# Optimization experiments

Hardware: AMD Instinct MI355X
Metric: run time of the kernel (lower is better)

Reference implementation:

```python
import jax, jax.numpy as jnp
import numpy as np

RADIUS = 8
NUM_CORNERS = 500


def _dwconv(x, k2d, mode):
    # depthwise 2D conv on NCHW with explicit border padding (kornia-style)
    ph, pw = k2d.shape[0] // 2, k2d.shape[1] // 2
    xp = jnp.pad(x, ((0, 0), (0, 0), (ph, ph), (pw, pw)), mode=mode)
    C = x.shape[1]
    kern = jnp.broadcast_to(k2d[None, None], (C, 1, k2d.shape[0], k2d.shape[1])).astype(x.dtype)
    return jax.lax.conv_general_dilated(xp, kern, (1, 1), 'VALID',
                                        feature_group_count=C,
                                        dimension_numbers=('NCHW', 'OIHW', 'NCHW'))


def _gauss2d(k, sigma):
    x = jnp.arange(k, dtype=jnp.float32) - (k - 1) / 2.0
    g = jnp.exp(-(x * x) / (2.0 * sigma * sigma))
    g = g / g.sum()
    return jnp.outer(g, g)


def _nms2d(x):
    # kornia.feature.nms2d with (5,5) window: keep values equal to local max
    m = jax.lax.reduce_window(x, -jnp.inf, jax.lax.max, (1, 1, 5, 5), (1, 1, 1, 1), 'SAME')
    return x * (x == m).astype(x.dtype)


def _gftt(gray):
    # kornia CornerGFTT: sobel gradients (normalized /8, replicate pad),
    # structure tensor blurred with gaussian(7, sigma=1), min eigenvalue
    kx = jnp.array([[-1., 0., 1.], [-2., 0., 2.], [-1., 0., 1.]], jnp.float32) / 8.0
    dx = _dwconv(gray, kx, 'edge')
    dy = _dwconv(gray, kx.T, 'edge')
    g7 = _gauss2d(7, 1.0)
    dx2 = _dwconv(dx * dx, g7, 'reflect')
    dy2 = _dwconv(dy * dy, g7, 'reflect')
    dxy = _dwconv(dx * dy, g7, 'reflect')
    det = dx2 * dy2 - dxy * dxy
    tr = dx2 + dy2
    return 0.5 * (tr - jnp.sqrt(jnp.abs(tr * tr - 4.0 * det)))


def _laplacian5(x):
    # kornia laplacian kernel size 5, normalized by abs-sum (=48), reflect pad
    k = jnp.ones((5, 5), jnp.float32).at[2, 2].set(1.0 - 25.0)
    k = k / jnp.abs(k).sum()
    return _dwconv(x, k, 'reflect')


def _get_corners(imgs):
    B, _, H, W = imgs.shape
    r, N = RADIUS, NUM_CORNERS
    gray = 0.299 * imgs[:, :1] + 0.587 * imgs[:, 1:2] + 0.114 * imgs[:, 2:3]
    corners = _nms2d(_gftt(gray))
    # MaxPool2d(r, return_indices) + MaxUnpool2d(r): keep only per-block max
    blocks = corners.reshape(B, 1, H // r, r, W // r, r)
    bmax = blocks.max(axis=(3, 5), keepdims=True)
    unpooled = jnp.where(blocks == bmax, blocks, 0.0).reshape(B, 1, H, W)
    values, idx = jax.lax.top_k(unpooled.reshape(B, -1), N)   # [B,N]
    h, w = idx // W, idx % W
    b = jnp.repeat(jnp.arange(B), N)
    target = jnp.zeros((B, 1, H, W), imgs.dtype).at[b, 0, h.ravel(), w.ravel()].set(values.ravel())
    target = _nms2d(target)
    return (target > 0).astype(target.dtype)


def setup_inputs() -> dict:
    key = jax.random.key(0)
    k1, k2 = jax.random.split(key)
    scores_dense = jax.random.uniform(k1, (16, 1, 512, 512), dtype=jnp.float32)
    imgs = jax.random.uniform(k2, (16, 3, 512, 512), dtype=jnp.float32)
    return {"scores_dense": scores_dense, "imgs": imgs}


def reference(scores_dense, imgs):
    corners = _dwconv(_get_corners(imgs), _gauss2d(7, 1.0), 'reflect')
    lap = _laplacian5(scores_dense)
    logp = jnp.clip(jnp.log(scores_dense), -100.0)      # torch BCELoss clamps log at -100
    log1mp = jnp.clip(jnp.log1p(-scores_dense), -100.0)
    bce = -(corners * logp + (1.0 - corners) * log1mp).mean()
    return bce + (scores_dense * jnp.exp(-lap)).mean() * 10.0
```

## Files before the change

kernel.cpp:

```cpp
#include <hip/hip_runtime.h>
#include <math.h>

#define BB 16
#define HH 512
#define WW 512
#define HWP (HH*WW)
#define NPIX (BB*HWP)
#define HWP4 (HWP/4)
#define NG (NPIX/4)
#define NCORN 500
#define NSLOT 4096
#define OCAP 1024
#define NKEY (NSLOT+OCAP)
#define NKPT (NKEY/256)
#define NBL 4096

__device__ __constant__ float G7c[7] = {
    0.0044330482f, 0.0540055826f, 0.2420362294f, 0.3990502793f,
    0.2420362294f, 0.0540055826f, 0.0044330482f};

__device__ __forceinline__ int reflect_idx(int i, int n) {
    if (i < 0) i = -i;
    if (i >= n) i = 2 * n - 2 - i;
    return i;
}

__device__ __forceinline__ float w1d(int p, int o, int n) {
    float w = 0.f;
    int d = p - o;
    if (d >= -3 && d <= 3) w += G7c[d + 3];
    if (p >= 1 && p + o <= 3) w += G7c[3 - p - o];
    if (p <= n - 2 && p + o >= 2 * n - 5) w += G7c[2 * n + 1 - p - o];
    return w;
}

__global__ void k_gray(const float* __restrict__ imgs, float* __restrict__ gray) {
    int g = blockIdx.x * blockDim.x + threadIdx.x;
    if (g >= NG) return;
    int b = g / HWP4, r = g % HWP4;
    const float4* base = (const float4*)(imgs + (size_t)b * 3 * HWP);
    float4 R = base[r], G = base[r + HWP4], Bc = base[r + 2 * HWP4];
    float4 o;
    o.x = 0.299f * R.x + 0.587f * G.x + 0.114f * Bc.x;
    o.y = 0.299f * R.y + 0.587f * G.y + 0.114f * Bc.y;
    o.z = 0.299f * R.z + 0.587f * G.z + 0.114f * Bc.z;
    o.w = 0.299f * R.w + 0.587f * G.w + 0.114f * Bc.w;
    ((float4*)gray)[g] = o;
}

__global__ void k_gradH(const float* __restrict__ gray,
                        float* __restrict__ ha, float* __restrict__ hc,
                        float* __restrict__ hd) {
    int g = blockIdx.x * blockDim.x + threadIdx.x;
    if (g >= NG) return;
    int b = g / HWP4, rem = g % HWP4;
    int p = rem * 4, y = p >> 9, x0 = p & 511;
    const float* gb = gray + (size_t)b * HWP;
    int ym = max(y - 1, 0), yp = min(y + 1, HH - 1);
    const float* rm = gb + (size_t)ym * WW;
    const float* rc = gb + (size_t)y * WW;
    const float* rp = gb + (size_t)yp * WW;
    if (x0 >= 4 && x0 <= 504) {
        float r0[12], r1[12], r2[12];
        const float4* q0 = (const float4*)(rm + x0 - 4);
        const float4* q1 = (const float4*)(rc + x0 - 4);
        const float4* q2 = (const float4*)(rp + x0 - 4);
#pragma unroll
        for (int t = 0; t < 3; ++t) {
            float4 a = q0[t], bq = q1[t], c = q2[t];
            r0[4*t]=a.x; r0[4*t+1]=a.y; r0[4*t+2]=a.z; r0[4*t+3]=a.w;
            r1[4*t]=bq.x; r1[4*t+1]=bq.y; r1[4*t+2]=bq.z; r1[4*t+3]=bq.w;
            r2[4*t]=c.x; r2[4*t+1]=c.y; r2[4*t+2]=c.z; r2[4*t+3]=c.w;
        }
        float dxv[10], dyv[10];
#pragma unroll
        for (int w = 1; w <= 10; ++w) {
            float dx = (r0[w+1]-r0[w-1] + 2.f*(r1[w+1]-r1[w-1]) + r2[w+1]-r2[w-1]) * 0.125f;
            float dy = (r2[w-1]-r0[w-1] + 2.f*(r2[w]-r0[w]) + r2[w+1]-r0[w+1]) * 0.125f;
            dxv[w-1] = dx; dyv[w-1] = dy;
        }
        float4 av, cv, dv;
        float* pa = (float*)&av; float* pc = (float*)&cv; float* pd = (float*)&dv;
#pragma unroll
        for (int k = 0; k < 4; ++k) {
            float a = 0.f, c = 0.f, d = 0.f;
#pragma unroll
            for (int t = -3; t <= 3; ++t) {
                int wi = k + 3 + t;
                float w = G7c[t + 3];
                a += w * dxv[wi] * dxv[wi];
                c += w * dyv[wi] * dyv[wi];
                d += w * dxv[wi] * dyv[wi];
            }
            pa[k] = a; pc[k] = c; pd[k] = d;
        }
        ((float4*)ha)[g] = av;
        ((float4*)hc)[g] = cv;
        ((float4*)hd)[g] = dv;
    } else {
        for (int k = 0; k < 4; ++k) {
            int x = x0 + k;
            float a = 0.f, c = 0.f, d = 0.f;
            for (int t = -3; t <= 3; ++t) {
                int xx = reflect_idx(x + t, WW);
                int xm = max(xx - 1, 0), xp = min(xx + 1, WW - 1);
                float g00 = rm[xm], g01 = rm[xx], g02 = rm[xp];
                float g10 = rc[xm],               g12 = rc[xp];
                float g20 = rp[xm], g21 = rp[xx], g22 = rp[xp];
                float dx = (g02 - g00 + 2.f * (g12 - g10) + g22 - g20) * 0.125f;
                float dy = (g20 - g00 + 2.f * (g21 - g01) + g22 - g02) * 0.125f;
                float w = G7c[t + 3];
                a += w * dx * dx; c += w * dy * dy; d += w * dx * dy;
            }
            size_t i = (size_t)b * HWP + p + k;
            ha[i] = a; hc[i] = c; hd[i] = d;
        }
    }
}

__global__ void k_gfttV(const float* __restrict__ ha, const float* __restrict__ hc,
                        const float* __restrict__ hd, float* __restrict__ S,
                        float* __restrict__ hm) {
    __shared__ float srow[1024];
    int b = blockIdx.x >> 8;
    int rp = blockIdx.x & 255;
    int half = threadIdx.x >> 7;
    int y = rp * 2 + half;
    int x0 = (threadIdx.x & 127) * 4;
    float4 a = {0,0,0,0}, c = {0,0,0,0}, d = {0,0,0,0};
#pragma unroll
    for (int j = -3; j <= 3; ++j) {
        int yy = reflect_idx(y + j, HH);
        float w = G7c[j + 3];
        size_t i4 = ((size_t)b * HWP + (size_t)yy * WW + x0) >> 2;
        float4 qa = ((const float4*)ha)[i4];
        float4 qc = ((const float4*)hc)[i4];
        float4 qd = ((const float4*)hd)[i4];
        a.x += w*qa.x; a.y += w*qa.y; a.z += w*qa.z; a.w += w*qa.w;
        c.x += w*qc.x; c.y += w*qc.y; c.z += w*qc.z; c.w += w*qc.w;
        d.x += w*qd.x; d.y += w*qd.y; d.z += w*qd.z; d.w += w*qd.w;
    }
    float4 o;
    float* pa = (float*)&a; float* pc = (float*)&c; float* pd = (float*)&d; float* po = (float*)&o;
#pragma unroll
    for (int k = 0; k < 4; ++k) {
        float det = pa[k] * pc[k] - pd[k] * pd[k];
        float tr = pa[k] + pc[k];
        po[k] = 0.5f * (tr - sqrtf(fabsf(tr * tr - 4.f * det)));
    }
    size_t g4 = ((size_t)b * HWP + (size_t)y * WW + x0) >> 2;
    ((float4*)S)[g4] = o;
    *((float4*)&srow[half * 512 + x0]) = o;
    __syncthreads();
    const float* row = &srow[half * 512];
    float4 hv; float* ph = (float*)&hv;
#pragma unroll
    for (int k = 0; k < 4; ++k) {
        int x = x0 + k;
        int xa = max(x - 2, 0), xb = min(x + 2, WW - 1);
        float m = -INFINITY;
        for (int xx = xa; xx <= xb; ++xx) m = fmaxf(m, row[xx]);
        ph[k] = m;
    }
    ((float4*)hm)[g4] = hv;
}

__global__ void k_cand(const float* __restrict__ hm, const float* __restrict__ S,
                       float* __restrict__ sval, int* __restrict__ sidx,
                       int* __restrict__ ocnt) {
    int wave = threadIdx.x >> 6, lane = threadIdx.x & 63;
    int tx = blockIdx.x * 4 + wave;
    int ty = blockIdx.y;
    int b = blockIdx.z;
    int ly = lane >> 3, lx = lane & 7;
    int y = ty * 8 + ly, x = tx * 8 + lx;
    const float* hb = hm + (size_t)b * HWP;
    int y0 = max(y - 2, 0), y1 = min(y + 2, HH - 1);
    float m = -INFINITY;
    for (int yy = y0; yy <= y1; ++yy) m = fmaxf(m, hb[yy * WW + x]);
    float v = S[(size_t)b * HWP + y * WW + x];
    float cval = (v == m) ? v : 0.f;
    float tm = cval;
#pragma unroll
    for (int off = 32; off; off >>= 1)
        tm = fmaxf(tm, __shfl_xor(tm, off));
    unsigned long long mask = __ballot(cval == tm && cval > 0.f);
    int slot = ty * 64 + tx;
    if (mask) {
        int first = __ffsll(mask) - 1;
        if (lane == first) {
            sval[b * NKEY + slot] = cval;
            sidx[b * NKEY + slot] = y * WW + x;
        } else if ((mask >> lane) & 1ull) {
            int pos = atomicAdd(&ocnt[b], 1);
            if (pos < OCAP) {
                sval[b * NKEY + NSLOT + pos] = cval;
                sidx[b * NKEY + NSLOT + pos] = y * WW + x;
            }
        }
    } else if (lane == 0) {
        sval[b * NKEY + slot] = 0.f;
        sidx[b * NKEY + slot] = 0;
    }
}

__global__ __launch_bounds__(256) void k_sel(const float* __restrict__ sval,
                       const int* __restrict__ sidx, const int* __restrict__ ocnt,
                       unsigned long long* __restrict__ selK) {
    __shared__ int shw[4];
    __shared__ int shtot;
    int b = blockIdx.x;
    int n = NSLOT + min(ocnt[b], OCAP);
    unsigned long long keys[NKPT];
    int cnt = 0;
#pragma unroll
    for (int t = 0; t < NKPT; ++t) {
        int i = threadIdx.x + t * 256;
        unsigned long long k = 0ull;
        if (i < n) {
            float v = sval[b * NKEY + i];
            if (v > 0.f) {
                unsigned int ix = (unsigned int)sidx[b * NKEY + i];
                k = ((unsigned long long)__float_as_uint(v) << 32) |
                    (unsigned long long)(~ix);
                cnt++;
            }
        }
        keys[t] = k;
    }
    int wid = threadIdx.x >> 6;
    {
        int c = cnt;
#pragma unroll
        for (int off = 32; off; off >>= 1) c += __shfl_down(c, off);
        if ((threadIdx.x & 63) == 0) shw[wid] = c;
        __syncthreads();
        if (threadIdx.x == 0) shtot = shw[0] + shw[1] + shw[2] + shw[3];
        __syncthreads();
    }
    int target = min(NCORN, shtot);
    unsigned long long T = 0ull;
    for (int bit = 63; bit >= 0; --bit) {
        unsigned long long cand = T | (1ull << bit);
        int c = 0;
#pragma unroll
        for (int t = 0; t < NKPT; ++t) c += (keys[t] >= cand) ? 1 : 0;
#pragma unroll
        for (int off = 32; off; off >>= 1) c += __shfl_down(c, off);
        __syncthreads();
        if ((threadIdx.x & 63) == 0) shw[wid] = c;
        __syncthreads();
        int tot = shw[0] + shw[1] + shw[2] + shw[3];
        if (tot >= target) T = cand;
    }
    if (threadIdx.x == 0) selK[b] = T;
}

__global__ void k_post(const float* __restrict__ sval, const int* __restrict__ sidx,
                       const int* __restrict__ ocnt, const unsigned long long* __restrict__ selK,
                       float* __restrict__ corners) {
    int gid = blockIdx.x * blockDim.x + threadIdx.x;
    if (gid >= BB * NKEY) return;
    int b = gid / NKEY, s = gid % NKEY;
    int novf = min(ocnt[b], OCAP);
    if (s >= NSLOT + novf) return;
    float v = sval[gid];
    if (v <= 0.f) return;
    unsigned int ix = (unsigned int)sidx[gid];
    unsigned long long K = selK[b];
    unsigned long long k = ((unsigned long long)__float_as_uint(v) << 32) |
                           (unsigned long long)(~ix);
    if (k < K) return;
    int y = (int)(ix >> 9), x = (int)(ix & 511);
    const float* bsv = sval + b * NKEY;
    const int* bsi = sidx + b * NKEY;
    bool sup = false;
    int ty0 = max(y - 2, 0) >> 3, ty1 = min(y + 2, HH - 1) >> 3;
    int tx0 = max(x - 2, 0) >> 3, tx1 = min(x + 2, WW - 1) >> 3;
    for (int ty = ty0; ty <= ty1 && !sup; ++ty)
        for (int tx = tx0; tx <= tx1 && !sup; ++tx) {
            int s2 = ty * 64 + tx;
            float v2 = bsv[s2];
            if (v2 <= v) continue;
            int ix2 = bsi[s2];
            unsigned long long k2 = ((unsigned long long)__float_as_uint(v2) << 32) |
                                    (unsigned long long)(~(unsigned int)ix2);
            if (k2 < K) continue;
            int y2 = ix2 >> 9, x2 = ix2 & 511;
            if (abs(y2 - y) <= 2 && abs(x2 - x) <= 2) sup = true;
        }
    for (int j = 0; j < novf && !sup; ++j) {
        float v2 = bsv[NSLOT + j];
        if (v2 <= v) continue;
        int ix2 = bsi[NSLOT + j];
        unsigned long long k2 = ((unsigned long long)__float_as_uint(v2) << 32) |
                                (unsigned long long)(~(unsigned int)ix2);
        if (k2 < K) continue;
        int y2 = ix2 >> 9, x2 = ix2 & 511;
        if (abs(y2 - y) <= 2 && abs(x2 - x) <= 2) sup = true;
    }
    if (sup) return;
    float* cb = corners + (size_t)b * HWP;
    if (y >= 3 && y <= HH - 4 && x >= 3 && x <= WW - 4) {
#pragma unroll
        for (int j = -3; j <= 3; ++j) {
            float wy = G7c[j + 3];
#pragma unroll
            for (int i = -3; i <= 3; ++i)
                atomicAdd(cb + (y + j) * WW + (x + i), wy * G7c[i + 3]);
        }
    } else {
        int oy0 = max(y - 6, 0), oy1 = min(y + 6, HH - 1);
        int ox0 = max(x - 6, 0), ox1 = min(x + 6, WW - 1);
        for (int oy = oy0; oy <= oy1; ++oy) {
            float wy = w1d(y, oy, HH);
            if (wy == 0.f) continue;
            for (int ox = ox0; ox <= ox1; ++ox) {
                float wx = w1d(x, ox, WW);
                if (wx != 0.f) atomicAdd(cb + oy * WW + ox, wy * wx);
            }
        }
    }
}

__global__ void k_loss(const float* __restrict__ scores, const float* __restrict__ corners,
                       float* __restrict__ partial) {
    int g = blockIdx.x * blockDim.x + threadIdx.x;
    float bce = 0.f, reg = 0.f;
    if (g < NG) {
        int b = g / HWP4, rem = g % HWP4;
        int p = rem * 4, y = p >> 9, x0 = p & 511;
        const float* sb = scores + (size_t)b * HWP;
        float s25[4] = {0.f, 0.f, 0.f, 0.f};
        float pv[4];
        if (x0 >= 4 && x0 <= 504) {
#pragma unroll
            for (int j = -2; j <= 2; ++j) {
                int yy = reflect_idx(y + j, HH);
                const float4* q = (const float4*)(sb + (size_t)yy * WW + x0 - 4);
                float4 qa = q[0], qb = q[1], qc = q[2];
                float f[12] = {qa.x,qa.y,qa.z,qa.w, qb.x,qb.y,qb.z,qb.w, qc.x,qc.y,qc.z,qc.w};
#pragma unroll
                for (int k = 0; k < 4; ++k)
                    s25[k] += f[k+2] + f[k+3] + f[k+4] + f[k+5] + f[k+6];
                if (j == 0) { pv[0]=f[4]; pv[1]=f[5]; pv[2]=f[6]; pv[3]=f[7]; }
            }
        } else {
            for (int k = 0; k < 4; ++k) {
                int x = x0 + k;
                float s = 0.f;
                for (int j = -2; j <= 2; ++j) {
                    const float* r = sb + (size_t)reflect_idx(y + j, HH) * WW;
                    for (int i = -2; i <= 2; ++i)
                        s += r[reflect_idx(x + i, WW)];
                }
                s25[k] = s;
                pv[k] = sb[(size_t)y * WW + x];
            }
        }
        float4 c4 = ((const float4*)corners)[g];
        float cv[4] = {c4.x, c4.y, c4.z, c4.w};
#pragma unroll
        for (int k = 0; k < 4; ++k) {
            float pp = pv[k], cc = cv[k];
            float lp = __logf(pp);
            lp = (lp > -100.f) ? lp : -100.f;
            float l1p = __logf(1.f - pp);
            l1p = (l1p > -100.f) ? l1p : -100.f;
            bce += -(cc * lp + (1.f - cc) * l1p);
            float lap = (s25[k] - 25.f * pp) * (1.0f / 48.0f);
            reg += pp * __expf(-lap);
        }
    }
#pragma unroll
    for (int off = 32; off; off >>= 1) {
        bce += __shfl_down(bce, off);
        reg += __shfl_down(reg, off);
    }
    __shared__ float wb[4], wr[4];
    int wid = threadIdx.x >> 6, lid = threadIdx.x & 63;
    if (lid == 0) { wb[wid] = bce; wr[wid] = reg; }
    __syncthreads();
    if (threadIdx.x == 0) {
        float tb = 0.f, tr = 0.f;
        for (int w = 0; w < 4; ++w) { tb += wb[w]; tr += wr[w]; }
        partial[blockIdx.x] = tb;
        partial[NBL + blockIdx.x] = tr;
    }
}

__global__ void k_reduce(const float* __restrict__ partial, float* __restrict__ out) {
    float tb = 0.f, tr = 0.f;
    for (int i = threadIdx.x; i < NBL; i += blockDim.x) {
        tb += partial[i];
        tr += partial[NBL + i];
    }
#pragma unroll
    for (int off = 32; off; off >>= 1) {
        tb += __shfl_down(tb, off);
        tr += __shfl_down(tr, off);
    }
    __shared__ float wb[4], wr[4];
    int wid = threadIdx.x >> 6, lid = threadIdx.x & 63;
    if (lid == 0) { wb[wid] = tb; wr[wid] = tr; }
    __syncthreads();
    if (threadIdx.x == 0) {
        float sb = 0.f, sr = 0.f;
        for (int w = 0; w < 4; ++w) { sb += wb[w]; sr += wr[w]; }
        float invN = 1.0f / (float)NPIX;
        out[0] = sb * invN + sr * invN * 10.0f;
    }
}

extern "C" void kernel_launch(void* const* d_in, const int* in_sizes, int n_in,
                              void* d_out, int out_size, void* d_ws, size_t ws_size,
                              hipStream_t stream) {
    const float* scores = (const float*)d_in[0];
    const float* imgs   = (const float*)d_in[1];
    float* out = (float*)d_out;

    float* ws = (float*)d_ws;
    float* A0 = ws;
    float* A1 = ws + (size_t)NPIX;
    float* A2 = ws + 2 * (size_t)NPIX;
    float* A3 = ws + 3 * (size_t)NPIX;
    float* sval = ws + 4 * (size_t)NPIX;
    int*   sidx = (int*)(sval + (size_t)BB * NKEY);
    int*   ocnt = (int*)(sidx + (size_t)BB * NKEY);
    unsigned long long* selK = (unsigned long long*)(ocnt + BB);
    float* partial = (float*)(selK + BB);

    const int T = 256;
    const int GG = NG / T;

    k_gray <<<GG, T, 0, stream>>>(imgs, A0);
    k_gradH<<<GG, T, 0, stream>>>(A0, A1, A2, A3);
    k_gfttV<<<BB * (HH / 2), 256, 0, stream>>>(A1, A2, A3, A0, A1);

    hipMemsetAsync(ocnt, 0, BB * sizeof(int), stream);
    dim3 gcand(16, 64, BB);
    k_cand<<<gcand, 256, 0, stream>>>(A1, A0, sval, sidx, ocnt);

    hipMemsetAsync(A2, 0, (size_t)NPIX * sizeof(float), stream);

    k_sel<<<BB, 256, 0, stream>>>(sval, sidx, ocnt, selK);
    const int GS = (BB * NKEY + T - 1) / T;
    k_post<<<GS, T, 0, stream>>>(sval, sidx, ocnt, selK, A2);

    k_loss  <<<NBL, T, 0, stream>>>(scores, A2, partial);
    k_reduce<<<1, 256, 0, stream>>>(partial, out);
}
```

Baseline: 329.9 us.

## Fuse gradient, structure tensor blur and GFTT into one banded kernel

Merges the horizontal gradient/blur kernel and the vertical blur/GFTT kernel into a single kernel where each thread owns a 4-wide column strip over an 8-row band. It recomputes the Sobel gradients for 14 source rows and accumulates the vertical Gaussian in registers, so the three full-size intermediate structure tensor planes are never written or read back. The candidate kernel now does the full 5x5 NMS from a shared-memory tile instead of reading a precomputed horizontal-max plane. In exchange the kernel does redundant gradient work on halo rows and needs many registers, which may reduce occupancy.

```diff
diff --git a/kernel.cpp b/kernel.cpp
--- a/kernel.cpp
+++ b/kernel.cpp
@@ -48,138 +48,139 @@
     ((float4*)gray)[g] = o;
 }
 
-__global__ void k_gradH(const float* __restrict__ gray,
-                        float* __restrict__ ha, float* __restrict__ hc,
-                        float* __restrict__ hd) {
-    int g = blockIdx.x * blockDim.x + threadIdx.x;
-    if (g >= NG) return;
-    int b = g / HWP4, rem = g % HWP4;
-    int p = rem * 4, y = p >> 9, x0 = p & 511;
+__global__ __launch_bounds__(256) void k_front(const float* __restrict__ gray,
+                                               float* __restrict__ S) {
+    int gid = blockIdx.x * 256 + threadIdx.x;
+    int cstrip = gid & 127;
+    int band = (gid >> 7) & 63;
+    int b = gid >> 13;
+    int x0 = cstrip * 4;
+    int y0 = band * 8;
     const float* gb = gray + (size_t)b * HWP;
-    int ym = max(y - 1, 0), yp = min(y + 1, HH - 1);
-    const float* rm = gb + (size_t)ym * WW;
-    const float* rc = gb + (size_t)y * WW;
-    const float* rp = gb + (size_t)yp * WW;
-    if (x0 >= 4 && x0 <= 504) {
-        float r0[12], r1[12], r2[12];
-        const float4* q0 = (const float4*)(rm + x0 - 4);
-        const float4* q1 = (const float4*)(rc + x0 - 4);
-        const float4* q2 = (const float4*)(rp + x0 - 4);
-#pragma unroll
-        for (int t = 0; t < 3; ++t) {
-            float4 a = q0[t], bq = q1[t], c = q2[t];
-            r0[4*t]=a.x; r0[4*t+1]=a.y; r0[4*t+2]=a.z; r0[4*t+3]=a.w;
-            r1[4*t]=bq.x; r1[4*t+1]=bq.y; r1[4*t+2]=bq.z; r1[4*t+3]=bq.w;
-            r2[4*t]=c.x; r2[4*t+1]=c.y; r2[4*t+2]=c.z; r2[4*t+3]=c.w;
-        }
-        float dxv[10], dyv[10];
-#pragma unroll
-        for (int w = 1; w <= 10; ++w) {
-            float dx = (r0[w+1]-r0[w-1] + 2.f*(r1[w+1]-r1[w-1]) + r2[w+1]-r2[w-1]) * 0.125f;
-            float dy = (r2[w-1]-r0[w-1] + 2.f*(r2[w]-r0[w]) + r2[w+1]-r0[w+1]) * 0.125f;
-            dxv[w-1] = dx; dyv[w-1] = dy;
-        }
-        float4 av, cv, dv;
-        float* pa = (float*)&av; float* pc = (float*)&cv; float* pd = (float*)&dv;
+    float* Sb = S + (size_t)b * HWP;
+    bool edgeL = (x0 == 0), edgeR = (x0 == 508);
+
+    float aA[7][4], aC[7][4], aD[7][4];
+#pragma unroll
+    for (int s = 0; s < 7; ++s)
+#pragma unroll
+        for (int k = 0; k < 4; ++k) { aA[s][k] = 0.f; aC[s][k] = 0.f; aD[s][k] = 0.f; }
+
+#pragma unroll
+    for (int i = 0; i < 14; ++i) {
+        int tp = y0 - 3 + i;
+        int src = reflect_idx(tp, HH);
+        int r0 = max(src - 1, 0), r2 = min(src + 1, HH - 1);
+        float G[3][12];
+        {
+            const float* rw0 = gb + (size_t)r0 * WW;
+            const float* rw1 = gb + (size_t)src * WW;
+            const float* rw2 = gb + (size_t)r2 * WW;
+            const float* rws[3] = {rw0, rw1, rw2};
+#pragma unroll
+            for (int r = 0; r < 3; ++r) {
+                const float* rw = rws[r];
+                float4 own = *(const float4*)(rw + x0);
+                G[r][4] = own.x; G[r][5] = own.y; G[r][6] = own.z; G[r][7] = own.w;
+                if (!edgeL) {
+                    float4 lf = *(const float4*)(rw + x0 - 4);
+                    G[r][0] = lf.x; G[r][1] = lf.y; G[r][2] = lf.z; G[r][3] = lf.w;
+                } else {
+                    G[r][0] = 0.f; G[r][1] = 0.f; G[r][2] = 0.f;
+                    G[r][3] = own.x;
+                }
+                if (!edgeR) {
+                    float4 rt = *(const float4*)(rw + x0 + 4);
+                    G[r][8] = rt.x; G[r][9] = rt.y; G[r][10] = rt.z; G[r][11] = rt.w;
+                } else {
+                    G[r][8] = own.w;
+                    G[r][9] = 0.f; G[r][10] = 0.f; G[r][11] = 0.f;
+                }
+            }
+        }
+        float pa[10], pc[10], pd[10];
+#pragma unroll
+        for (int j = 0; j < 10; ++j) {
+            int gi = j + 1;
+            float dx = (G[0][gi+1] - G[0][gi-1] + 2.f * (G[1][gi+1] - G[1][gi-1])
+                        + G[2][gi+1] - G[2][gi-1]) * 0.125f;
+            float dy = (G[2][gi-1] - G[0][gi-1] + 2.f * (G[2][gi] - G[0][gi])
+                        + G[2][gi+1] - G[0][gi+1]) * 0.125f;
+            pa[j] = dx * dx; pc[j] = dy * dy; pd[j] = dx * dy;
+        }
+        if (edgeL) {
+            pa[2] = pa[4]; pc[2] = pc[4]; pd[2] = pd[4];
+            pa[1] = pa[5]; pc[1] = pc[5]; pd[1] = pd[5];
+            pa[0] = pa[6]; pc[0] = pc[6]; pd[0] = pd[6];
+        }
+        if (edgeR) {
+            pa[7] = pa[5]; pc[7] = pc[5]; pd[7] = pd[5];
+            pa[8] = pa[4]; pc[8] = pc[4]; pd[8] = pd[4];
+            pa[9] = pa[3]; pc[9] = pc[3]; pd[9] = pd[3];
+        }
+        float hA[4], hC[4], hD[4];
 #pragma unroll
         for (int k = 0; k < 4; ++k) {
-            float a = 0.f, c = 0.f, d = 0.f;
-#pragma unroll
-            for (int t = -3; t <= 3; ++t) {
-                int wi = k + 3 + t;
-                float w = G7c[t + 3];
-                a += w * dxv[wi] * dxv[wi];
-                c += w * dyv[wi] * dyv[wi];
-                d += w * dxv[wi] * dyv[wi];
-            }
-            pa[k] = a; pc[k] = c; pd[k] = d;
-        }
-        ((float4*)ha)[g] = av;
-        ((float4*)hc)[g] = cv;
-        ((float4*)hd)[g] = dv;
-    } else {
-        for (int k = 0; k < 4; ++k) {
-            int x = x0 + k;
-            float a = 0.f, c = 0.f, d = 0.f;
-            for (int t = -3; t <= 3; ++t) {
-                int xx = reflect_idx(x + t, WW);
-                int xm = max(xx - 1, 0), xp = min(xx + 1, WW - 1);
-                float g00 = rm[xm], g01 = rm[xx], g02 = rm[xp];
-                float g10 = rc[xm],               g12 = rc[xp];
-                float g20 = rp[xm], g21 = rp[xx], g22 = rp[xp];
-                float dx = (g02 - g00 + 2.f * (g12 - g10) + g22 - g20) * 0.125f;
-                float dy = (g20 - g00 + 2.f * (g21 - g01) + g22 - g02) * 0.125f;
-                float w = G7c[t + 3];
-                a += w * dx * dx; c += w * dy * dy; d += w * dx * dy;
-            }
-            size_t i = (size_t)b * HWP + p + k;
-            ha[i] = a; hc[i] = c; hd[i] = d;
-        }
-    }
-}
-
-__global__ void k_gfttV(const float* __restrict__ ha, const float* __restrict__ hc,
-                        const float* __restrict__ hd, float* __restrict__ S,
-                        float* __restrict__ hm) {
-    __shared__ float srow[1024];
-    int b = blockIdx.x >> 8;
-    int rp = blockIdx.x & 255;
-    int half = threadIdx.x >> 7;
-    int y = rp * 2 + half;
-    int x0 = (threadIdx.x & 127) * 4;
-    float4 a = {0,0,0,0}, c = {0,0,0,0}, d = {0,0,0,0};
-#pragma unroll
-    for (int j = -3; j <= 3; ++j) {
-        int yy = reflect_idx(y + j, HH);
-        float w = G7c[j + 3];
-        size_t i4 = ((size_t)b * HWP + (size_t)yy * WW + x0) >> 2;
-        float4 qa = ((const float4*)ha)[i4];
-        float4 qc = ((const float4*)hc)[i4];
-        float4 qd = ((const float4*)hd)[i4];
-        a.x += w*qa.x; a.y += w*qa.y; a.z += w*qa.z; a.w += w*qa.w;
-        c.x += w*qc.x; c.y += w*qc.y; c.z += w*qc.z; c.w += w*qc.w;
-        d.x += w*qd.x; d.y += w*qd.y; d.z += w*qd.z; d.w += w*qd.w;
-    }
-    float4 o;
-    float* pa = (float*)&a; float* pc = (float*)&c; float* pd = (float*)&d; float* po = (float*)&o;
-#pragma unroll
-    for (int k = 0; k < 4; ++k) {
-        float det = pa[k] * pc[k] - pd[k] * pd[k];
-        float tr = pa[k] + pc[k];
-        po[k] = 0.5f * (tr - sqrtf(fabsf(tr * tr - 4.f * det)));
-    }
-    size_t g4 = ((size_t)b * HWP + (size_t)y * WW + x0) >> 2;
-    ((float4*)S)[g4] = o;
-    *((float4*)&srow[half * 512 + x0]) = o;
-    __syncthreads();
-    const float* row = &srow[half * 512];
-    float4 hv; float* ph = (float*)&hv;
-#pragma unroll
-    for (int k = 0; k < 4; ++k) {
-        int x = x0 + k;
-        int xa = max(x - 2, 0), xb = min(x + 2, WW - 1);
-        float m = -INFINITY;
-        for (int xx = xa; xx <= xb; ++xx) m = fmaxf(m, row[xx]);
-        ph[k] = m;
-    }
-    ((float4*)hm)[g4] = hv;
-}
-
-__global__ void k_cand(const float* __restrict__ hm, const float* __restrict__ S,
-                       float* __restrict__ sval, int* __restrict__ sidx,
-                       int* __restrict__ ocnt) {
+            float A = 0.f, C = 0.f, D = 0.f;
+#pragma unroll
+            for (int t = 0; t < 7; ++t) {
+                float w = G7c[t];
+                A += w * pa[k + t]; C += w * pc[k + t]; D += w * pd[k + t];
+            }
+            hA[k] = A; hC[k] = C; hD[k] = D;
+        }
+#pragma unroll
+        for (int d2 = 0; d2 < 7; ++d2) {
+            int l = i - 6 + d2;
+            if (l < 0 || l > 7) continue;
+            float w = G7c[6 - d2];
+#pragma unroll
+            for (int k = 0; k < 4; ++k) {
+                aA[l % 7][k] += w * hA[k];
+                aC[l % 7][k] += w * hC[k];
+                aD[l % 7][k] += w * hD[k];
+            }
+        }
+        if (i >= 6) {
+            int l = i - 6, s = l % 7;
+            float4 o; float* po = (float*)&o;
+#pragma unroll
+            for (int k = 0; k < 4; ++k) {
+                float det = aA[s][k] * aC[s][k] - aD[s][k] * aD[s][k];
+                float tr = aA[s][k] + aC[s][k];
+                po[k] = 0.5f * (tr - sqrtf(fabsf(tr * tr - 4.f * det)));
+                aA[s][k] = 0.f; aC[s][k] = 0.f; aD[s][k] = 0.f;
+            }
+            *(float4*)(Sb + (size_t)(y0 + l) * WW + x0) = o;
+        }
+    }
+}
+
+__global__ void k_cand2(const float* __restrict__ S, float* __restrict__ sval,
+                        int* __restrict__ sidx, int* __restrict__ ocnt) {
+    __shared__ float tile[4][12][12];
     int wave = threadIdx.x >> 6, lane = threadIdx.x & 63;
     int tx = blockIdx.x * 4 + wave;
     int ty = blockIdx.y;
     int b = blockIdx.z;
+    const float* sb = S + (size_t)b * HWP;
+    for (int t = lane; t < 144; t += 64) {
+        int r = t / 12, c = t % 12;
+        int yy = min(max(ty * 8 - 2 + r, 0), HH - 1);
+        int xx = min(max(tx * 8 - 2 + c, 0), WW - 1);
+        tile[wave][r][c] = sb[yy * WW + xx];
+    }
+    __syncthreads();
     int ly = lane >> 3, lx = lane & 7;
+    float v = tile[wave][ly + 2][lx + 2];
+    float m = -INFINITY;
+#pragma unroll
+    for (int dy = 0; dy < 5; ++dy)
+#pragma unroll
+        for (int dx = 0; dx < 5; ++dx)
+            m = fmaxf(m, tile[wave][ly + dy][lx + dx]);
+    float cval = (v == m) ? v : 0.f;
     int y = ty * 8 + ly, x = tx * 8 + lx;
-    const float* hb = hm + (size_t)b * HWP;
-    int y0 = max(y - 2, 0), y1 = min(y + 2, HH - 1);
-    float m = -INFINITY;
-    for (int yy = y0; yy <= y1; ++yy) m = fmaxf(m, hb[yy * WW + x]);
-    float v = S[(size_t)b * HWP + y * WW + x];
-    float cval = (v == m) ? v : 0.f;
     float tm = cval;
 #pragma unroll
     for (int off = 32; off; off >>= 1)
@@ -423,8 +424,7 @@
     float* A0 = ws;
     float* A1 = ws + (size_t)NPIX;
     float* A2 = ws + 2 * (size_t)NPIX;
-    float* A3 = ws + 3 * (size_t)NPIX;
-    float* sval = ws + 4 * (size_t)NPIX;
+    float* sval = ws + 3 * (size_t)NPIX;
     int*   sidx = (int*)(sval + (size_t)BB * NKEY);
     int*   ocnt = (int*)(sidx + (size_t)BB * NKEY);
     unsigned long long* selK = (unsigned long long*)(ocnt + BB);
@@ -434,12 +434,11 @@
     const int GG = NG / T;
 
     k_gray <<<GG, T, 0, stream>>>(imgs, A0);
-    k_gradH<<<GG, T, 0, stream>>>(A0, A1, A2, A3);
-    k_gfttV<<<BB * (HH / 2), 256, 0, stream>>>(A1, A2, A3, A0, A1);
+    k_front<<<BB * 64 * 128 / T, T, 0, stream>>>(A0, A1);
 
     hipMemsetAsync(ocnt, 0, BB * sizeof(int), stream);
     dim3 gcand(16, 64, BB);
-    k_cand<<<gcand, 256, 0, stream>>>(A1, A0, sval, sidx, ocnt);
+    k_cand2<<<gcand, 256, 0, stream>>>(A1, sval, sidx, ocnt);
 
     hipMemsetAsync(A2, 0, (size_t)NPIX * sizeof(float), stream);
 
```

New measurement: 293.6 us. -11.0%, faster.
